# Kernel tuning notes

Hardware: AMD Instinct MI355X
Metric: run time of the kernel (lower is better)

## Reference

```python
import jax, jax.numpy as jnp
import numpy as np

N_NODES = 50000
N_EDGES = 500000
D_FEAT = 128
HIDDEN = 128
EPS = 1e-8


def _lin_init(key, fan_in, fan_out):
    return jax.random.normal(key, (fan_in, fan_out), dtype=jnp.float32) / np.sqrt(fan_in)


def setup_inputs() -> dict:
    key = jax.random.key(0)
    ks = jax.random.split(key, 16)
    h = jax.random.normal(ks[0], (N_NODES, D_FEAT), dtype=jnp.float32)
    coord = jax.random.normal(ks[1], (N_NODES, 3), dtype=jnp.float32)
    vel = jax.random.normal(ks[2], (N_NODES, 3), dtype=jnp.float32)
    edge_index = jax.random.randint(ks[3], (2, N_EDGES), 0, N_NODES, dtype=jnp.int32)
    return {
        "h": h, "coord": coord, "vel": vel, "edge_index": edge_index,
        "W_e1": _lin_init(ks[4], 2 * D_FEAT + 1, HIDDEN), "b_e1": jnp.zeros((HIDDEN,), jnp.float32),
        "W_e2": _lin_init(ks[5], HIDDEN, D_FEAT), "b_e2": jnp.zeros((D_FEAT,), jnp.float32),
        "W_c1": _lin_init(ks[6], D_FEAT, HIDDEN), "b_c1": jnp.zeros((HIDDEN,), jnp.float32),
        "W_c2": _lin_init(ks[7], HIDDEN, 1), "b_c2": jnp.zeros((1,), jnp.float32),
        "W_v1": _lin_init(ks[8], D_FEAT, HIDDEN), "b_v1": jnp.zeros((HIDDEN,), jnp.float32),
        "W_v2": _lin_init(ks[9], HIDDEN, 1), "b_v2": jnp.zeros((1,), jnp.float32),
        "W_n1": _lin_init(ks[10], 2 * D_FEAT, HIDDEN), "b_n1": jnp.zeros((HIDDEN,), jnp.float32),
        "W_n2": _lin_init(ks[11], HIDDEN, D_FEAT), "b_n2": jnp.zeros((D_FEAT,), jnp.float32),
    }


def reference(h, coord, vel, edge_index,
              W_e1, b_e1, W_e2, b_e2,
              W_c1, b_c1, W_c2, b_c2,
              W_v1, b_v1, W_v2, b_v2,
              W_n1, b_n1, W_n2, b_n2):
    act = jax.nn.silu
    r, c = edge_index[0], edge_index[1]
    n = coord.shape[0]

    # coord2radial with normalize=True
    diff = coord[r] - coord[c]                      # [E, 3]
    rad = jnp.sum(diff * diff, axis=-1, keepdims=True)  # [E, 1]
    norm = jnp.sqrt(jax.lax.stop_gradient(rad)) + EPS
    diff = diff / norm

    # edge_op: Linear -> act -> Linear -> act
    edge_in = jnp.concatenate([h[r], h[c], rad], axis=1)  # [E, 2D+1]
    m_ij = act(act(edge_in @ W_e1 + b_e1) @ W_e2 + b_e2)  # [E, D]

    # coord_op: Linear -> act -> Linear (scalar weight per edge)
    weights = act(m_ij @ W_c1 + b_c1) @ W_c2 + b_c2       # [E, 1]
    coors_sum = jax.ops.segment_sum(diff * weights, r, num_segments=n)  # [N, 3]

    # vel_op: Linear -> act -> Linear (scalar per node)
    vel_weights = act(h @ W_v1 + b_v1) @ W_v2 + b_v2      # [N, 1]
    coord_out = coord + coors_sum + vel * vel_weights

    # node aggregation + node_op: Linear -> act -> Linear
    m_i = jax.ops.segment_sum(m_ij, r, num_segments=h.shape[0])  # [N, D]
    agg = jnp.concatenate([h, m_i], axis=1)               # [N, 2D]
    h_out = act(agg @ W_n1 + b_n1) @ W_n2 + b_n2          # [N, D]
    return (h_out, coord_out)
```

## Files before the change

### kernel.cpp

```cpp
#include <hip/hip_runtime.h>
#include <stdint.h>

#define NN 50000
#define NE 500000
#define BLK 256
#define NEB ((NE + 127) / 128)
#define SST 136

#define BARRIER() asm volatile("s_waitcnt lgkmcnt(0)\n\ts_barrier" ::: "memory")

typedef __attribute__((ext_vector_type(8))) short bf16x8;
typedef __attribute__((ext_vector_type(4))) float f32x4;

__device__ __forceinline__ float silu(float x) { return x / (1.0f + __expf(-x)); }
__device__ __forceinline__ float bf2f(unsigned short s) {
    union { unsigned int u; float f; } v; v.u = ((unsigned int)s) << 16; return v.f;
}
__device__ __forceinline__ unsigned short f2bf(float f) {
    union { float f; unsigned int u; } v; v.f = f;
    return (unsigned short)((v.u + 0x7fffu + ((v.u >> 16) & 1u)) >> 16);
}
__device__ __forceinline__ unsigned int pack2(float a, float b) {
    return (unsigned int)f2bf(a) | ((unsigned int)f2bf(b) << 16);
}
__device__ __forceinline__ bf16x8 packf8(const float* p) {
    float4 f0 = *(const float4*)p; float4 f1 = *(const float4*)(p + 4);
    union { bf16x8 v; unsigned int u[4]; } o;
    o.u[0] = pack2(f0.x, f0.y); o.u[1] = pack2(f0.z, f0.w);
    o.u[2] = pack2(f1.x, f1.y); o.u[3] = pack2(f1.z, f1.w);
    return o.v;
}

__global__ void prep_h(const float* __restrict__ h, unsigned short* __restrict__ hb) {
    int i = blockIdx.x * 256 + threadIdx.x;
    if (i < NN * 128 / 4) {
        float4 v = ((const float4*)h)[i];
        uint2 o; o.x = pack2(v.x, v.y); o.y = pack2(v.z, v.w);
        ((uint2*)hb)[i] = o;
    }
}

__global__ void prep_w(const float* __restrict__ We1, const float* __restrict__ We2,
                       const float* __restrict__ Wc1, const float* __restrict__ Wv1,
                       const float* __restrict__ Wn1, const float* __restrict__ Wn2,
                       unsigned short* __restrict__ Wt1, unsigned short* __restrict__ Wt2,
                       unsigned short* __restrict__ Wt3, unsigned short* __restrict__ Wv1t,
                       unsigned short* __restrict__ Wn1t, unsigned short* __restrict__ Wn2t) {
    int i = blockIdx.x * 256 + threadIdx.x;
    if (i < 32768) {
        int j = i >> 8, k = i & 255;
        Wt1[i] = f2bf(We1[k * 128 + j]);
    } else if (i < 49152) {
        int t = i - 32768; int j = t >> 7, ks = t & 127;
        int k0 = (ks & 7) * 16 + (ks >> 3);
        Wt2[t] = f2bf(We2[k0 * 128 + j]);
    } else if (i < 65536) {
        int t = i - 49152; int j = t >> 7, ks = t & 127;
        int k0 = (ks & 7) * 16 + (ks >> 3);
        Wt3[t] = f2bf(Wc1[k0 * 128 + j]);
    } else if (i < 81920) {
        int t = i - 65536; int j = t >> 7, k = t & 127;
        Wv1t[t] = f2bf(Wv1[k * 128 + j]);
    } else if (i < 114688) {
        int t = i - 81920; int j = t >> 8, k = t & 255;
        int ksrc;
        if (k < 128) ksrc = k;
        else { int ks = k - 128; ksrc = 128 + (ks & 7) * 16 + (ks >> 3); }
        Wn1t[t] = f2bf(Wn1[ksrc * 128 + j]);
    } else if (i < 131072) {
        int t = i - 114688; int j = t >> 7, ks = t & 127;
        int k0 = (ks & 7) * 16 + (ks >> 3);
        Wn2t[t] = f2bf(Wn2[k0 * 128 + j]);
    }
}

__global__ void csr_count(const int* __restrict__ eidx, int* __restrict__ deg) {
    int e = blockIdx.x * 256 + threadIdx.x;
    if (e < NE) atomicAdd(&deg[eidx[e]], 1);
}

__global__ void scan_a(const int* __restrict__ deg, int* __restrict__ bsum) {
    __shared__ int s[256];
    int t = threadIdx.x, idx = blockIdx.x * 256 + t;
    s[t] = (idx < NN) ? deg[idx] : 0;
    __syncthreads();
    for (int off = 128; off > 0; off >>= 1) {
        if (t < off) s[t] += s[t + off];
        __syncthreads();
    }
    if (t == 0) bsum[blockIdx.x] = s[0];
}

__global__ void scan_b(int* __restrict__ bsum) {
    __shared__ int s[256];
    int t = threadIdx.x;
    int v = (t < 196) ? bsum[t] : 0;
    s[t] = v;
    __syncthreads();
    for (int off = 1; off < 256; off <<= 1) {
        int x = (t >= off) ? s[t - off] : 0;
        __syncthreads();
        s[t] += x;
        __syncthreads();
    }
    if (t < 196) bsum[t] = s[t] - v;
}

__global__ void scan_c(const int* __restrict__ deg, const int* __restrict__ bsum,
                       int* __restrict__ rowptr) {
    __shared__ int s[256];
    int t = threadIdx.x, idx = blockIdx.x * 256 + t;
    int v = (idx < NN) ? deg[idx] : 0;
    s[t] = v;
    __syncthreads();
    for (int off = 1; off < 256; off <<= 1) {
        int x = (t >= off) ? s[t - off] : 0;
        __syncthreads();
        s[t] += x;
        __syncthreads();
    }
    if (idx < NN) rowptr[idx] = bsum[blockIdx.x] + s[t] - v;
    if (idx == 0) rowptr[NN] = NE;
}

__global__ void csr_fill(const int* __restrict__ eidx, const int* __restrict__ rowptr,
                         int* __restrict__ cursor,
                         int* __restrict__ csr_r, int* __restrict__ csr_c) {
    int e = blockIdx.x * 256 + threadIdx.x;
    if (e < NE) {
        int r = eidx[e], c = eidx[NE + e];
        int slot = rowptr[r] + atomicAdd(&cursor[r], 1);
        csr_r[slot] = r; csr_c[slot] = c;
    }
}

__device__ __forceinline__ void wpref256(const unsigned short* __restrict__ W, int halfk,
                                         uint4 w[8], int tid) {
#pragma unroll
    for (int t = 0; t < 8; ++t) {
        int idx = tid + t * 256; int j = idx >> 4, g = idx & 15;
        w[t] = *(const uint4*)(W + (size_t)j * 256 + halfk * 128 + g * 8);
    }
}
__device__ __forceinline__ void wpref128(const unsigned short* __restrict__ W,
                                         uint4 w[8], int tid) {
#pragma unroll
    for (int t = 0; t < 8; ++t) {
        int idx = tid + t * 256; int j = idx >> 4, g = idx & 15;
        w[t] = *(const uint4*)(W + (size_t)j * 128 + g * 8);
    }
}
__device__ __forceinline__ void wwrite(const uint4 w[8], unsigned short* sW, int tid) {
#pragma unroll
    for (int t = 0; t < 8; ++t) {
        int idx = tid + t * 256; int j = idx >> 4, g = idx & 15;
        *(uint4*)(sW + j * SST + g * 8) = w[t];
    }
}
__device__ __forceinline__ void mfma4(const bf16x8 a[2][4], const unsigned short* sW,
                                      int l16, int q, f32x4 acc[2][8]) {
#pragma unroll
    for (int kc = 0; kc < 4; ++kc)
#pragma unroll
        for (int ct = 0; ct < 8; ++ct) {
            bf16x8 b = *(const bf16x8*)(sW + (ct * 16 + l16) * SST + kc * 32 + q * 8);
            acc[0][ct] = __builtin_amdgcn_mfma_f32_16x16x32_bf16(a[0][kc], b, acc[0][ct], 0, 0, 0);
            acc[1][ct] = __builtin_amdgcn_mfma_f32_16x16x32_bf16(a[1][kc], b, acc[1][ct], 0, 0, 0);
        }
}

__global__ __launch_bounds__(BLK, 2) void egcl_edge(
    const float* __restrict__ coord,
    const int* __restrict__ csr_r, const int* __restrict__ csr_c,
    const unsigned short* __restrict__ hb,
    const unsigned short* __restrict__ Wt1,
    const unsigned short* __restrict__ Wt2,
    const unsigned short* __restrict__ Wt3,
    const float* __restrict__ We1,
    const float* __restrict__ be1, const float* __restrict__ be2,
    const float* __restrict__ bc1,
    const float* __restrict__ Wc2, const float* __restrict__ bc2,
    float* __restrict__ m_acc, float* __restrict__ c_sum)
{
    __shared__ __align__(16) unsigned short sAb[128 * SST];
    __shared__ __align__(16) unsigned short sW[128 * SST];
    __shared__ float sRad[128], sDif[128][3];
    __shared__ int sSeg[128];
    __shared__ float sBe1[128], sBe2[128], sBc1[128], sWlast[128], sWc2f[128];

    const int tid = threadIdx.x;
    const int wv = tid >> 6, lane = tid & 63, q = lane >> 4, l16 = lane & 15;
    const int e0 = blockIdx.x * 128;

    int nr[2], nc[2];
#pragma unroll
    for (int si = 0; si < 2; ++si) {
        int e = e0 + (wv * 2 + si) * 16 + l16;
        if (e >= NE) e = NE - 1;
        nr[si] = csr_r[e]; nc[si] = csr_c[e];
    }

    if (tid < 128) {
        sBe1[tid] = be1[tid]; sBe2[tid] = be2[tid]; sBc1[tid] = bc1[tid];
        sWlast[tid] = We1[256 * 128 + tid]; sWc2f[tid] = Wc2[tid];
        int s = e0 + tid; int sc = (s < NE) ? s : (NE - 1);
        int r = csr_r[sc], c = csr_c[sc];
        sSeg[tid] = (s < NE) ? r : -1;
        float dx = coord[r * 3 + 0] - coord[c * 3 + 0];
        float dy = coord[r * 3 + 1] - coord[c * 3 + 1];
        float dz = coord[r * 3 + 2] - coord[c * 3 + 2];
        float rad = fmaf(dx, dx, fmaf(dy, dy, dz * dz));
        float inv = 1.0f / (sqrtf(rad) + 1e-8f);
        sRad[tid] = rad;
        sDif[tid][0] = dx * inv; sDif[tid][1] = dy * inv; sDif[tid][2] = dz * inv;
    }

    uint4 w[8];
    wpref256(Wt1, 0, w, tid);
    wwrite(w, sW, tid);

    bf16x8 ar[2][4], ac[2][4];
#pragma unroll
    for (int si = 0; si < 2; ++si)
#pragma unroll
        for (int kc = 0; kc < 4; ++kc) {
            ar[si][kc] = *(const bf16x8*)(hb + (size_t)nr[si] * 128 + kc * 32 + q * 8);
            ac[si][kc] = *(const bf16x8*)(hb + (size_t)nc[si] * 128 + kc * 32 + q * 8);
        }
    wpref256(Wt1, 1, w, tid);
    const float bc2v = bc2[0];
    BARRIER();

    f32x4 acc[2][8];
#pragma unroll
    for (int si = 0; si < 2; ++si)
#pragma unroll
        for (int ct = 0; ct < 8; ++ct) acc[si][ct] = (f32x4){0.f, 0.f, 0.f, 0.f};

    mfma4(ar, sW, l16, q, acc);
    BARRIER();
    wwrite(w, sW, tid);
    wpref128(Wt2, w, tid);
    BARRIER();
    mfma4(ac, sW, l16, q, acc);
    BARRIER();
    wwrite(w, sW, tid);
    wpref128(Wt3, w, tid);

#pragma unroll
    for (int si = 0; si < 2; ++si)
#pragma unroll
        for (int r = 0; r < 4; ++r) {
            int row = (wv * 2 + si) * 16 + q * 4 + r;
            float rad = sRad[row];
            float v[8];
#pragma unroll
            for (int ct = 0; ct < 8; ++ct) {
                int col = ct * 16 + l16;
                v[ct] = silu(acc[si][ct][r] + rad * sWlast[col] + sBe1[col]);
            }
            uint4 pk = make_uint4(pack2(v[0], v[1]), pack2(v[2], v[3]),
                                  pack2(v[4], v[5]), pack2(v[6], v[7]));
            *(uint4*)(sAb + row * SST + l16 * 8) = pk;
        }
    BARRIER();

#pragma unroll
    for (int si = 0; si < 2; ++si)
#pragma unroll
        for (int ct = 0; ct < 8; ++ct) acc[si][ct] = (f32x4){0.f, 0.f, 0.f, 0.f};
    {
        bf16x8 a[2][4];
#pragma unroll
        for (int si = 0; si < 2; ++si) {
            int row = (wv * 2 + si) * 16 + l16;
#pragma unroll
            for (int kc = 0; kc < 4; ++kc)
                a[si][kc] = *(const bf16x8*)(sAb + row * SST + kc * 32 + q * 8);
        }
        mfma4(a, sW, l16, q, acc);
    }
    uint4 mu[2][4];
#pragma unroll
    for (int si = 0; si < 2; ++si)
#pragma unroll
        for (int r = 0; r < 4; ++r) {
            float v[8];
#pragma unroll
            for (int ct = 0; ct < 8; ++ct) v[ct] = silu(acc[si][ct][r] + sBe2[ct * 16 + l16]);
            mu[si][r] = make_uint4(pack2(v[0], v[1]), pack2(v[2], v[3]),
                                   pack2(v[4], v[5]), pack2(v[6], v[7]));
        }
    BARRIER();
#pragma unroll
    for (int si = 0; si < 2; ++si)
#pragma unroll
        for (int r = 0; r < 4; ++r) {
            int row = (wv * 2 + si) * 16 + q * 4 + r;
            *(uint4*)(sAb + row * SST + l16 * 8) = mu[si][r];
        }
    wwrite(w, sW, tid);
    BARRIER();

#pragma unroll
    for (int si = 0; si < 2; ++si)
#pragma unroll
        for (int ct = 0; ct < 8; ++ct) acc[si][ct] = (f32x4){0.f, 0.f, 0.f, 0.f};
    {
        bf16x8 a[2][4];
#pragma unroll
        for (int si = 0; si < 2; ++si) {
            int row = (wv * 2 + si) * 16 + l16;
#pragma unroll
            for (int kc = 0; kc < 4; ++kc)
                a[si][kc] = *(const bf16x8*)(sAb + row * SST + kc * 32 + q * 8);
        }
        mfma4(a, sW, l16, q, acc);
    }
#pragma unroll
    for (int si = 0; si < 2; ++si) {
        float p[4];
#pragma unroll
        for (int r = 0; r < 4; ++r) {
            float s = 0.f;
#pragma unroll
            for (int ct = 0; ct < 8; ++ct) {
                int col = ct * 16 + l16;
                float t = silu(acc[si][ct][r] + sBc1[col]);
                s = fmaf(t, sWc2f[col], s);
            }
            p[r] = s;
        }
#pragma unroll
        for (int m = 1; m < 16; m <<= 1)
#pragma unroll
            for (int r = 0; r < 4; ++r) p[r] += __shfl_xor(p[r], m, 16);
        if (l16 == 0) {
#pragma unroll
            for (int r = 0; r < 4; ++r) {
                int row = (wv * 2 + si) * 16 + q * 4 + r;
                int rn = sSeg[row];
                if (rn >= 0) {
                    float wgt = p[r] + bc2v;
                    atomicAdd(&c_sum[(size_t)rn * 3 + 0], sDif[row][0] * wgt);
                    atomicAdd(&c_sum[(size_t)rn * 3 + 1], sDif[row][1] * wgt);
                    atomicAdd(&c_sum[(size_t)rn * 3 + 2], sDif[row][2] * wgt);
                }
            }
        }
    }

    {
        int p = tid & 127, half = tid >> 7;
        int base = half * 64;
        float run = 0.f;
        int cur = sSeg[base];
        bool openL = true;
#pragma unroll 1
        for (int i = 0; i < 64; ++i) {
            int row = base + i;
            int rr = sSeg[row];
            if (rr != cur) {
                if (cur >= 0) {
                    float* dst = &m_acc[(size_t)cur * 128 + p];
                    if (openL) atomicAdd(dst, run);
                    else       *dst = run;
                }
                run = 0.f; cur = rr; openL = false;
            }
            run += bf2f(sAb[row * SST + p]);
        }
        if (cur >= 0) atomicAdd(&m_acc[(size_t)cur * 128 + p], run);
    }
}

__global__ __launch_bounds__(BLK, 3) void egcl_node(
    const unsigned short* __restrict__ hb,
    const float* __restrict__ coord,
    const float* __restrict__ vel,
    const unsigned short* __restrict__ Wv1t, const float* __restrict__ bv1,
    const float* __restrict__ Wv2, const float* __restrict__ bv2,
    const unsigned short* __restrict__ Wn1t, const float* __restrict__ bn1,
    const unsigned short* __restrict__ Wn2t, const float* __restrict__ bn2,
    const float* __restrict__ m_acc, const float* __restrict__ c_sum,
    float* __restrict__ out_h, float* __restrict__ out_c)
{
    __shared__ __align__(16) unsigned short sAb[128 * SST];
    __shared__ float sBv1[128], sWv2f[128], sBn1[128], sBn2[128];

    const int tid = threadIdx.x;
    const int wv = tid >> 6, lane = tid & 63, q = lane >> 4, l16 = lane & 15;
    const int n0 = blockIdx.x * 128;
    int nval = NN - n0; if (nval > 128) nval = 128;

    if (tid < 128) {
        sBv1[tid] = bv1[tid]; sWv2f[tid] = Wv2[tid];
        sBn1[tid] = bn1[tid]; sBn2[tid] = bn2[tid];
    }
    const float bv2v = bv2[0];

    bf16x8 ah[2][4], am[2][4];
#pragma unroll
    for (int si = 0; si < 2; ++si) {
        int row = (wv * 2 + si) * 16 + l16;
        int nn = n0 + row; if (nn >= NN) nn = NN - 1;
#pragma unroll
        for (int kc = 0; kc < 4; ++kc) {
            ah[si][kc] = *(const bf16x8*)(hb + (size_t)nn * 128 + kc * 32 + q * 8);
            am[si][kc] = packf8(m_acc + (size_t)nn * 128 + kc * 32 + q * 8);
        }
    }

    BARRIER();

    f32x4 acc[2][8];
#pragma unroll
    for (int si = 0; si < 2; ++si)
#pragma unroll
        for (int ct = 0; ct < 8; ++ct) acc[si][ct] = (f32x4){0.f, 0.f, 0.f, 0.f};
#pragma unroll
    for (int kc = 0; kc < 4; ++kc)
#pragma unroll
        for (int ct = 0; ct < 8; ++ct) {
            bf16x8 b = *(const bf16x8*)(Wv1t + (size_t)(ct * 16 + l16) * 128 + kc * 32 + q * 8);
            acc[0][ct] = __builtin_amdgcn_mfma_f32_16x16x32_bf16(ah[0][kc], b, acc[0][ct], 0, 0, 0);
            acc[1][ct] = __builtin_amdgcn_mfma_f32_16x16x32_bf16(ah[1][kc], b, acc[1][ct], 0, 0, 0);
        }
#pragma unroll
    for (int si = 0; si < 2; ++si) {
        float p[4];
#pragma unroll
        for (int r = 0; r < 4; ++r) {
            float s = 0.f;
#pragma unroll
            for (int ct = 0; ct < 8; ++ct) {
                int col = ct * 16 + l16;
                float t = silu(acc[si][ct][r] + sBv1[col]);
                s = fmaf(t, sWv2f[col], s);
            }
            p[r] = s;
        }
#pragma unroll
        for (int m = 1; m < 16; m <<= 1)
#pragma unroll
            for (int r = 0; r < 4; ++r) p[r] += __shfl_xor(p[r], m, 16);
        if (l16 == 0) {
#pragma unroll
            for (int r = 0; r < 4; ++r) {
                int row = (wv * 2 + si) * 16 + q * 4 + r;
                int n = n0 + row;
                if (row < nval) {
                    float vw = p[r] + bv2v;
#pragma unroll
                    for (int d = 0; d < 3; ++d) {
                        float cv = coord[(size_t)n * 3 + d] + c_sum[(size_t)n * 3 + d]
                                 + vel[(size_t)n * 3 + d] * vw;
                        out_c[(size_t)n * 3 + d] = cv;
                    }
                }
            }
        }
    }

#pragma unroll
    for (int si = 0; si < 2; ++si)
#pragma unroll
        for (int ct = 0; ct < 8; ++ct) acc[si][ct] = (f32x4){0.f, 0.f, 0.f, 0.f};
#pragma unroll
    for (int kc = 0; kc < 8; ++kc)
#pragma unroll
        for (int ct = 0; ct < 8; ++ct) {
            bf16x8 b = *(const bf16x8*)(Wn1t + (size_t)(ct * 16 + l16) * 256 + kc * 32 + q * 8);
            bf16x8 a0 = (kc < 4) ? ah[0][kc & 3] : am[0][kc & 3];
            bf16x8 a1 = (kc < 4) ? ah[1][kc & 3] : am[1][kc & 3];
            acc[0][ct] = __builtin_amdgcn_mfma_f32_16x16x32_bf16(a0, b, acc[0][ct], 0, 0, 0);
            acc[1][ct] = __builtin_amdgcn_mfma_f32_16x16x32_bf16(a1, b, acc[1][ct], 0, 0, 0);
        }
#pragma unroll
    for (int si = 0; si < 2; ++si)
#pragma unroll
        for (int r = 0; r < 4; ++r) {
            int row = (wv * 2 + si) * 16 + q * 4 + r;
            float v[8];
#pragma unroll
            for (int ct = 0; ct < 8; ++ct) v[ct] = silu(acc[si][ct][r] + sBn1[ct * 16 + l16]);
            uint4 pk = make_uint4(pack2(v[0], v[1]), pack2(v[2], v[3]),
                                  pack2(v[4], v[5]), pack2(v[6], v[7]));
            *(uint4*)(sAb + row * SST + l16 * 8) = pk;
        }

    BARRIER();

#pragma unroll
    for (int si = 0; si < 2; ++si)
#pragma unroll
        for (int ct = 0; ct < 8; ++ct) acc[si][ct] = (f32x4){0.f, 0.f, 0.f, 0.f};
    {
        bf16x8 a[2][4];
#pragma unroll
        for (int si = 0; si < 2; ++si) {
            int row = (wv * 2 + si) * 16 + l16;
#pragma unroll
            for (int kc = 0; kc < 4; ++kc)
                a[si][kc] = *(const bf16x8*)(sAb + row * SST + kc * 32 + q * 8);
        }
#pragma unroll
        for (int kc = 0; kc < 4; ++kc)
#pragma unroll
            for (int ct = 0; ct < 8; ++ct) {
                bf16x8 b = *(const bf16x8*)(Wn2t + (size_t)(ct * 16 + l16) * 128 + kc * 32 + q * 8);
                acc[0][ct] = __builtin_amdgcn_mfma_f32_16x16x32_bf16(a[0][kc], b, acc[0][ct], 0, 0, 0);
                acc[1][ct] = __builtin_amdgcn_mfma_f32_16x16x32_bf16(a[1][kc], b, acc[1][ct], 0, 0, 0);
            }
    }
#pragma unroll
    for (int si = 0; si < 2; ++si)
#pragma unroll
        for (int r = 0; r < 4; ++r) {
            int row = (wv * 2 + si) * 16 + q * 4 + r;
            if (row < nval) {
                float* orow = out_h + (size_t)(n0 + row) * 128;
#pragma unroll
                for (int ct = 0; ct < 8; ++ct)
                    orow[ct * 16 + l16] = acc[si][ct][r] + sBn2[ct * 16 + l16];
            }
        }
}

extern "C" void kernel_launch(void* const* d_in, const int* in_sizes, int n_in,
                              void* d_out, int out_size, void* d_ws, size_t ws_size,
                              hipStream_t stream) {
    const float* h     = (const float*)d_in[0];
    const float* coord = (const float*)d_in[1];
    const float* vel   = (const float*)d_in[2];
    const int*   eidx  = (const int*)d_in[3];
    const float* We1 = (const float*)d_in[4];
    const float* be1 = (const float*)d_in[5];
    const float* We2 = (const float*)d_in[6];
    const float* be2 = (const float*)d_in[7];
    const float* Wc1 = (const float*)d_in[8];
    const float* bc1 = (const float*)d_in[9];
    const float* Wc2 = (const float*)d_in[10];
    const float* bc2 = (const float*)d_in[11];
    const float* Wv1 = (const float*)d_in[12];
    const float* bv1 = (const float*)d_in[13];
    const float* Wv2 = (const float*)d_in[14];
    const float* bv2 = (const float*)d_in[15];
    const float* Wn1 = (const float*)d_in[16];
    const float* bn1 = (const float*)d_in[17];
    const float* Wn2 = (const float*)d_in[18];
    const float* bn2 = (const float*)d_in[19];

    char* ws = (char*)d_ws;
    float* m_acc = (float*)ws;
    float* c_sum = (float*)(ws + 25600000);
    unsigned short* hb   = (unsigned short*)(ws + 26200064);
    unsigned short* Wt1  = (unsigned short*)(ws + 39000064);
    unsigned short* Wt2  = (unsigned short*)(ws + 39065600);
    unsigned short* Wt3  = (unsigned short*)(ws + 39098368);
    unsigned short* Wv1t = (unsigned short*)(ws + 39131136);
    unsigned short* Wn1t = (unsigned short*)(ws + 39163904);
    unsigned short* Wn2t = (unsigned short*)(ws + 39229440);
    int* deg    = (int*)(ws + 39262208);
    int* cursor = (int*)(ws + 39462208);
    int* rowptr = (int*)(ws + 39662208);
    int* bsum   = (int*)(ws + 39862272);
    int* csr_r  = (int*)(ws + 39863296);
    int* csr_c  = (int*)(ws + 41863296);

    hipMemsetAsync(ws, 0, 26200000, stream);
    hipMemsetAsync(ws + 39262208, 0, 400000, stream);

    prep_h<<<6250, 256, 0, stream>>>(h, hb);
    prep_w<<<512, 256, 0, stream>>>(We1, We2, Wc1, Wv1, Wn1, Wn2,
                                    Wt1, Wt2, Wt3, Wv1t, Wn1t, Wn2t);

    csr_count<<<1954, 256, 0, stream>>>(eidx, deg);
    scan_a<<<196, 256, 0, stream>>>(deg, bsum);
    scan_b<<<1, 256, 0, stream>>>(bsum);
    scan_c<<<196, 256, 0, stream>>>(deg, bsum, rowptr);
    csr_fill<<<1954, 256, 0, stream>>>(eidx, rowptr, cursor, csr_r, csr_c);

    egcl_edge<<<NEB, BLK, 0, stream>>>(
        coord, csr_r, csr_c, hb, Wt1, Wt2, Wt3,
        We1, be1, be2, bc1, Wc2, bc2, m_acc, c_sum);

    float* out_h = (float*)d_out;
    float* out_c = out_h + (size_t)NN * 128;
    egcl_node<<<(NN + 127) / 128, BLK, 0, stream>>>(
        hb, coord, vel, Wv1t, bv1, Wv2, bv2, Wn1t, bn1, Wn2t, bn2,
        m_acc, c_sum, out_h, out_c);
}
```

Measured before the change: 457.4 us.

## Double-buffer first-layer weights in LDS, use hardware bf16 pack, batch segment reads

After: 414.5 us. -9.4%, faster.

```diff
diff --git a/kernel.cpp b/kernel.cpp
--- a/kernel.cpp
+++ b/kernel.cpp
@@ -21,7 +21,9 @@
     return (unsigned short)((v.u + 0x7fffu + ((v.u >> 16) & 1u)) >> 16);
 }
 __device__ __forceinline__ unsigned int pack2(float a, float b) {
-    return (unsigned int)f2bf(a) | ((unsigned int)f2bf(b) << 16);
+    unsigned int r;
+    asm("v_cvt_pk_bf16_f32 %0, %1, %2" : "=v"(r) : "v"(a), "v"(b));
+    return r;
 }
 __device__ __forceinline__ bf16x8 packf8(const float* p) {
     float4 f0 = *(const float4*)p; float4 f1 = *(const float4*)(p + 4);
@@ -215,10 +217,9 @@
         sDif[tid][0] = dx * inv; sDif[tid][1] = dy * inv; sDif[tid][2] = dz * inv;
     }
 
-    uint4 w[8];
-    wpref256(Wt1, 0, w, tid);
-    wwrite(w, sW, tid);
-
+    uint4 wA[8], wB[8];
+    wpref256(Wt1, 0, wA, tid);
+    wpref256(Wt1, 1, wB, tid);
     bf16x8 ar[2][4], ac[2][4];
 #pragma unroll
     for (int si = 0; si < 2; ++si)
@@ -227,7 +228,9 @@
             ar[si][kc] = *(const bf16x8*)(hb + (size_t)nr[si] * 128 + kc * 32 + q * 8);
             ac[si][kc] = *(const bf16x8*)(hb + (size_t)nc[si] * 128 + kc * 32 + q * 8);
         }
-    wpref256(Wt1, 1, w, tid);
+    wwrite(wA, sW, tid);
+    wwrite(wB, sAb, tid);
+    wpref128(Wt2, wA, tid);
     const float bc2v = bc2[0];
     BARRIER();
 
@@ -238,14 +241,10 @@
         for (int ct = 0; ct < 8; ++ct) acc[si][ct] = (f32x4){0.f, 0.f, 0.f, 0.f};
 
     mfma4(ar, sW, l16, q, acc);
-    BARRIER();
-    wwrite(w, sW, tid);
-    wpref128(Wt2, w, tid);
-    BARRIER();
-    mfma4(ac, sW, l16, q, acc);
-    BARRIER();
-    wwrite(w, sW, tid);
-    wpref128(Wt3, w, tid);
+    mfma4(ac, sAb, l16, q, acc);
+    BARRIER();
+    wwrite(wA, sW, tid);
+    wpref128(Wt3, wA, tid);
 
 #pragma unroll
     for (int si = 0; si < 2; ++si)
@@ -280,7 +279,6 @@
         }
         mfma4(a, sW, l16, q, acc);
     }
-    uint4 mu[2][4];
 #pragma unroll
     for (int si = 0; si < 2; ++si)
 #pragma unroll
@@ -288,18 +286,13 @@
             float v[8];
 #pragma unroll
             for (int ct = 0; ct < 8; ++ct) v[ct] = silu(acc[si][ct][r] + sBe2[ct * 16 + l16]);
-            mu[si][r] = make_uint4(pack2(v[0], v[1]), pack2(v[2], v[3]),
-                                   pack2(v[4], v[5]), pack2(v[6], v[7]));
-        }
-    BARRIER();
-#pragma unroll
-    for (int si = 0; si < 2; ++si)
-#pragma unroll
-        for (int r = 0; r < 4; ++r) {
             int row = (wv * 2 + si) * 16 + q * 4 + r;
-            *(uint4*)(sAb + row * SST + l16 * 8) = mu[si][r];
-        }
-    wwrite(w, sW, tid);
+            *(uint4*)(sAb + row * SST + l16 * 8) =
+                make_uint4(pack2(v[0], v[1]), pack2(v[2], v[3]),
+                           pack2(v[4], v[5]), pack2(v[6], v[7]));
+        }
+    BARRIER();
+    wwrite(wA, sW, tid);
     BARRIER();
 
 #pragma unroll
@@ -357,18 +350,26 @@
         int cur = sSeg[base];
         bool openL = true;
 #pragma unroll 1
-        for (int i = 0; i < 64; ++i) {
-            int row = base + i;
-            int rr = sSeg[row];
-            if (rr != cur) {
-                if (cur >= 0) {
-                    float* dst = &m_acc[(size_t)cur * 128 + p];
-                    if (openL) atomicAdd(dst, run);
-                    else       *dst = run;
+        for (int i0 = 0; i0 < 64; i0 += 4) {
+            float v[4]; int rr[4];
+#pragma unroll
+            for (int j = 0; j < 4; ++j) {
+                int row = base + i0 + j;
+                rr[j] = sSeg[row];
+                v[j] = bf2f(sAb[row * SST + p]);
+            }
+#pragma unroll
+            for (int j = 0; j < 4; ++j) {
+                if (rr[j] != cur) {
+                    if (cur >= 0) {
+                        float* dst = &m_acc[(size_t)cur * 128 + p];
+                        if (openL) atomicAdd(dst, run);
+                        else       *dst = run;
+                    }
+                    run = 0.f; cur = rr[j]; openL = false;
                 }
-                run = 0.f; cur = rr; openL = false;
-            }
-            run += bf2f(sAb[row * SST + p]);
+                run += v[j];
+            }
         }
         if (cur >= 0) atomicAdd(&m_acc[(size_t)cur * 128 + p], run);
     }
```
